# Kernel optimization log

Measured on AMD Instinct MI355X. Metric: run time of the kernel, lower is better.

## Reference

```python
import jax, jax.numpy as jnp
import numpy as np

# ---------------- irreps metadata: list of (mul, l, parity) ----------------
IR_A  = [(1, 0, 1)]                                        # '0e' input scalars
IR_B  = [(10,0,1),(10,0,-1),(10,0,1),(5,1,1),(5,1,-1)]     # Gate input, dim 60
IR_C  = [(10,0,1),(10,0,-1),(5,1,1),(5,1,-1)]              # Gate output, dim 50
IR_D  = [(1,0,-1),(6,0,1)]                                 # '0o + 6x0e', dim 7
IR_SH = [(1,0,1),(1,1,-1)]                                 # '0e + 1o'
CONVS = [(IR_A,IR_B),(IR_C,IR_B),(IR_C,IR_B),(IR_C,IR_B),(IR_C,IR_D)]
R_BASIS  = 2
DIAMETER = 5.0   # source used 1.5 -> degenerate 1^3 kernel; enlarged to exercise the steerable conv
STEP     = 1.0

def irdim(ir):
    return sum(m*(2*l+1) for m,l,_ in ir)

def irslices(ir):
    out, o = [], 0
    for m,l,_ in ir:
        d = m*(2*l+1); out.append(slice(o,o+d)); o += d
    return out

# normalized Clebsch-Gordan (wigner3j * sqrt(2*l_out+1)) for l<=1
_eps = np.zeros((3,3,3))
for a,b,c in [(0,1,2),(1,2,0),(2,0,1)]:
    _eps[a,b,c] = 1.0; _eps[b,a,c] = -1.0
CG = {
    (0,0,0): np.ones((1,1,1)),
    (0,1,1): np.eye(3).reshape(1,3,3),
    (1,0,1): np.eye(3).reshape(3,1,3),
    (1,1,0): (np.eye(3)/np.sqrt(3.0)).reshape(3,3,1),
    (1,1,1): _eps/np.sqrt(2.0),
}

def tp_ins(ir1, iro):
    ins = []
    for i1,(m1,l1,p1) in enumerate(ir1):
        for i2,(m2,l2,p2) in enumerate(IR_SH):
            for io,(mo,lo,po) in enumerate(iro):
                if po == p1*p2 and abs(l1-l2) <= lo <= l1+l2:
                    ins.append((i1,i2,io))
    return ins

def tp_numel(ir1, iro):
    return sum(R_BASIS*ir1[i1][0]*IR_SH[i2][0]*iro[io][0] for i1,i2,io in tp_ins(ir1,iro))

def lin_ins(ir1, iro):
    return [(i,j) for i,(m1,l1,p1) in enumerate(ir1)
                  for j,(m2,l2,p2) in enumerate(iro) if l1==l2 and p1==p2]

def lin_numel(ir1, iro):
    return sum(ir1[i][0]*iro[j][0] for i,j in lin_ins(ir1,iro))

def _lattice_features():
    # lattice offsets, smooth_finite radial basis (with cutoff) and SH ('0e+1o', component norm)
    r = DIAMETER/2.0
    s = int(np.floor(r/STEP))
    c = np.arange(-s, s+1, dtype=np.float64)*STEP
    lat = np.stack(np.meshgrid(c, c, c, indexing='ij'), -1)            # [K,K,K,3]
    d = np.linalg.norm(lat, axis=-1)
    vals = np.linspace(0.0, r, R_BASIS+2)[1:-1]
    step = vals[1]-vals[0]
    diff = (d[...,None]-vals)/step
    sus = lambda t: np.where(t>0, np.exp(-1.0/np.where(t>0, t, 1.0)), 0.0)
    emb = 1.14136*np.exp(2.0)*sus(diff+1.0)*sus(1.0-diff)              # [K,K,K,R]
    unit = lat/np.maximum(d, 1e-9)[...,None]
    sh = np.concatenate([np.ones_like(d)[...,None],
                         np.sqrt(3.0)*unit[...,[1,2,0]]], -1)          # [K,K,K,4], e3nn (y,z,x) order
    return jnp.asarray(emb, jnp.float32), jnp.asarray(sh, jnp.float32)

EMB, SH = _lattice_features()

def build_kernel(ir_in, ir_out, tw, lw):
    sin, sout, ssh = irslices(ir_in), irslices(ir_out), irslices(IR_SH)
    K = EMB.shape[0]
    k = jnp.zeros((K, K, K, irdim(ir_in), irdim(ir_out)), jnp.float32)
    off = 0
    for i1,i2,io in tp_ins(ir_in, ir_out):
        m1,l1,_ = ir_in[i1]; m2,l2,_ = IR_SH[i2]; mo,lo,_ = ir_out[io]
        n = R_BASIS*m1*m2*mo
        w = tw[off:off+n].reshape(R_BASIS, m1, mo); off += n           # m2 == 1 for SH
        cg = jnp.asarray(CG[(l1,l2,lo)], jnp.float32)
        alpha = 1.0/np.sqrt(m1*m2*R_BASIS)
        shseg = SH[..., ssh[i2]]                                       # [K,K,K,2l2+1]
        blk = alpha*jnp.einsum('xyzr,ruw,xyzj,ijk->xyzuiwk', EMB, w, shseg, cg)
        k = k.at[:,:,:, sin[i1], sout[io]].add(
            blk.reshape(K, K, K, m1*(2*l1+1), mo*(2*lo+1)))
    # self-connection Linear at the kernel center (radial basis vanishes at r=0)
    M = jnp.zeros((irdim(ir_in), irdim(ir_out)), jnp.float32)
    off = 0
    for i,j in lin_ins(ir_in, ir_out):
        m1,l1,_ = ir_in[i]; mo,_,_ = ir_out[j]
        w = lw[off:off+m1*mo].reshape(m1, mo); off += m1*mo
        eye = jnp.eye(2*l1+1, dtype=jnp.float32)
        blk = (1.0/np.sqrt(m1))*jnp.einsum('uw,ik->uiwk', w, eye)
        M = M.at[sin[i], sout[j]].add(blk.reshape(m1*(2*l1+1), mo*(2*l1+1)))
    cc = K//2
    return k.at[cc, cc, cc].set(M)

def equiv_conv(x, k):
    return jax.lax.conv_general_dilated(x, k, (1,1,1), 'SAME',
        dimension_numbers=('NXYZC', 'XYZIO', 'NXYZC'))

def gate(y):
    # Gate('10x0e+10x0o', [gelu, tanh], '10x0e', [sigmoid], '5x1e+5x1o')
    s = jnp.concatenate([jax.nn.gelu(y[..., :10]), jnp.tanh(y[..., 10:20])], -1)
    g = jax.nn.sigmoid(y[..., 20:30])                                  # 10 gate scalars
    v = y[..., 30:60].reshape(y.shape[:-1]+(10,3))*g[..., None]        # gate 5x1e + 5x1o
    return jnp.concatenate([s, v.reshape(y.shape[:-1]+(30,))], -1)

def _forward(x, tws, lws):
    y = x
    for i,(a,b) in enumerate(CONVS):
        y = equiv_conv(y, build_kernel(a, b, tws[i], lws[i]))
        if i < len(CONVS)-1:
            y = gate(y)
    return jnp.sum(y, axis=(1, 2, 3))                                  # [B, 7]

def setup_inputs() -> dict:
    key = jax.random.key(0)
    ks = jax.random.split(key, 11)
    inp = {'x': jax.random.normal(ks[0], (2, 48, 48, 48, 1), jnp.float32)}
    for i,(a,b) in enumerate(CONVS):
        inp[f'tp_w{i}'] = jax.random.normal(ks[1+i], (tp_numel(a,b),), jnp.float32)
        inp[f'lin_w{i}'] = jax.random.normal(ks[6+i], (lin_numel(a,b),), jnp.float32)
    return inp

def reference(x, tp_w0, tp_w1, tp_w2, tp_w3, tp_w4,
              lin_w0, lin_w1, lin_w2, lin_w3, lin_w4):
    return _forward(x, [tp_w0, tp_w1, tp_w2, tp_w3, tp_w4],
                    [lin_w0, lin_w1, lin_w2, lin_w3, lin_w4])
```

## Files before the change

### kernel.cpp

```cpp
#include <hip/hip_runtime.h>
#include <hip/hip_bf16.h>
#include <math.h>


typedef __attribute__((ext_vector_type(8))) short bf16x8;
typedef __attribute__((ext_vector_type(4))) float f32x4;

struct TpPath { int off, ci, co, m1, l1, i2, mo, lo; float alpha; };
struct LinPath { int off, ci, co, m1, l, mo; float norm; };

__device__ __constant__ TpPath g_tp[19] = {
  {0,  0,  0, 1, 0, 0, 10, 0, 0.70710678f},
  {20, 0, 20, 1, 0, 0, 10, 0, 0.70710678f},
  {40, 0, 45, 1, 0, 1,  5, 1, 0.70710678f},
  {0,    0,  0, 10, 0, 0, 10, 0, 0.22360680f},
  {200,  0, 20, 10, 0, 0, 10, 0, 0.22360680f},
  {400,  0, 45, 10, 0, 1,  5, 1, 0.22360680f},
  {500, 10, 10, 10, 0, 0, 10, 0, 0.22360680f},
  {700, 10, 30, 10, 0, 1,  5, 1, 0.22360680f},
  {800, 20, 30,  5, 1, 0,  5, 1, 0.31622777f},
  {850, 20, 10,  5, 1, 1, 10, 0, 0.31622777f},
  {950, 20, 45,  5, 1, 1,  5, 1, 0.31622777f},
  {1000,35, 45,  5, 1, 0,  5, 1, 0.31622777f},
  {1050,35,  0,  5, 1, 1, 10, 0, 0.31622777f},
  {1150,35, 20,  5, 1, 1, 10, 0, 0.31622777f},
  {1250,35, 30,  5, 1, 1,  5, 1, 0.31622777f},
  {0,    0, 1, 10, 0, 0, 6, 0, 0.22360680f},
  {120, 10, 0, 10, 0, 0, 1, 0, 0.22360680f},
  {140, 20, 0,  5, 1, 1, 1, 0, 0.31622777f},
  {150, 35, 1,  5, 1, 1, 6, 0, 0.31622777f},
};

__device__ __constant__ LinPath g_lin[9] = {
  {0,  0,  0, 1, 0, 10, 1.0f},
  {10, 0, 20, 1, 0, 10, 1.0f},
  {0,   0,  0, 10, 0, 10, 0.31622777f},
  {100, 0, 20, 10, 0, 10, 0.31622777f},
  {200,10, 10, 10, 0, 10, 0.31622777f},
  {300,20, 30,  5, 1,  5, 0.44721360f},
  {325,35, 45,  5, 1,  5, 0.44721360f},
  {0,  0, 1, 10, 0, 6, 0.31622777f},
  {60,10, 0, 10, 0, 1, 0.31622777f},
};

__device__ inline float sus_f(float t) { return t > 0.f ? __expf(-1.f / t) : 0.f; }

__global__ void build_tp_kernel(const float* __restrict__ tw, float* __restrict__ kbuf,
                                int CIN, int COUT, int path_base) {
  TpPath p = g_tp[path_base + blockIdx.x];
  const int dl1 = 2 * p.l1 + 1, dlo = 2 * p.lo + 1;
  const int du = p.m1 * dl1, dw = p.mo * dlo;
  const int total = 125 * du * dw;
  const float C0 = 1.14136f * expf(2.0f);
  for (int e = threadIdx.x; e < total; e += blockDim.x) {
    int xyz = e / (du * dw);
    int rem = e % (du * dw);
    int ui = rem / dw, wk = rem % dw;
    int u = ui / dl1, i = ui % dl1;
    int w = wk / dlo, kk = wk % dlo;
    int kx = xyz / 25, ky = (xyz / 5) % 5, kz = xyz % 5;
    float cx = (float)(kx - 2), cy = (float)(ky - 2), cz = (float)(kz - 2);
    float d = sqrtf(cx * cx + cy * cy + cz * cz);
    float t = 1.2f * d;
    float e0 = C0 * sus_f(t) * sus_f(2.f - t);
    float e1 = C0 * sus_f(t - 1.f) * sus_f(3.f - t);
    float radial = e0 * tw[p.off + (0 * p.m1 + u) * p.mo + w] +
                   e1 * tw[p.off + (1 * p.m1 + u) * p.mo + w];
    float invd = (d > 0.f) ? 1.f / d : 0.f;
    const float s3 = 1.7320508f;
    float sh1[3] = { s3 * cy * invd, s3 * cz * invd, s3 * cx * invd };
    float shfac;
    if (p.l1 == 0 && p.i2 == 0)      shfac = 1.f;
    else if (p.l1 == 0)              shfac = sh1[kk];
    else if (p.i2 == 0)              shfac = (i == kk) ? 1.f : 0.f;
    else if (p.lo == 0)              shfac = sh1[i] * 0.57735027f;
    else {
      if (i == kk) shfac = 0.f;
      else {
        int j = 3 - i - kk;
        float sgn = (j == (i + 1) % 3) ? 1.f : -1.f;
        shfac = sgn * sh1[j] * 0.70710678f;
      }
    }
    kbuf[(size_t)(xyz * CIN + p.ci + ui) * COUT + p.co + wk] = p.alpha * radial * shfac;
  }
}

__global__ void set_center_kernel(const float* __restrict__ lw, float* __restrict__ kbuf,
                                  int CIN, int COUT, int lin_base, int nlin) {
  for (int l = 0; l < nlin; l++) {
    LinPath q = g_lin[lin_base + l];
    int dl = 2 * q.l + 1;
    int tot = q.m1 * q.mo * dl;
    for (int e = threadIdx.x; e < tot; e += blockDim.x) {
      int u = e / (q.mo * dl);
      int r = e % (q.mo * dl);
      int w = r / dl, ii = r % dl;
      kbuf[(size_t)(62 * CIN + q.ci + u * dl + ii) * COUT + q.co + w * dl + ii] =
          q.norm * lw[q.off + u * q.mo + w];
    }
  }
}

__global__ void convert_w(const float* __restrict__ kbuf, unsigned short* __restrict__ kwbT,
                          int CIN, int COUT) {
  int idx = blockIdx.x * 256 + threadIdx.x;
  if (idx >= 125 * 64 * 64) return;
  int tap = idx >> 12, co = (idx >> 6) & 63, ci = idx & 63;
  float v = (ci < CIN && co < COUT) ? kbuf[((size_t)tap * CIN + ci) * COUT + co] : 0.f;
  __hip_bfloat16 h = __float2bfloat16(v);
  kwbT[idx] = *(unsigned short*)&h;
}

__global__ void build_w0(const float* __restrict__ k0, unsigned short* __restrict__ wb0L) {
  int idx = blockIdx.x * 256 + threadIdx.x;
  if (idx >= 5 * 2 * 64 * 32) return;
  int k = idx & 31, co = (idx >> 5) & 63, mf = (idx >> 11) & 1, dxi = idx >> 12;
  float v = 0.f;
  if (co < 60) {
    if (mf == 0) {
      int dy = k >> 3, dz = k & 7;
      if (dz < 5) v = k0[(size_t)(((dxi * 5 + dy) * 5 + dz)) * 60 + co];
    } else {
      int kg = k >> 3, dz = k & 7;
      if (kg == 0 && dz < 5) v = k0[(size_t)(((dxi * 5 + 4) * 5 + dz)) * 60 + co];
    }
  }
  __hip_bfloat16 h = __float2bfloat16(v);
  wb0L[idx] = *(unsigned short*)&h;
}

__device__ inline float gelu_f(float x) {
  float inner = 0.79788456f * (x + 0.044715f * x * x * x);
  return 0.5f * x * (1.f + tanhf(inner));
}
__device__ inline float sigm_f(float x) { return 1.f / (1.f + __expf(-x)); }

__device__ inline void gate_tile(const float* my, unsigned int* myO, int z) {
#pragma unroll
  for (int p = 0; p < 25; p++) {
    float a0, a1;
    if (p < 5) {
      a0 = gelu_f(my[(2 * p) * 16 + z]);
      a1 = gelu_f(my[(2 * p + 1) * 16 + z]);
    } else if (p < 10) {
      a0 = tanhf(my[(2 * p) * 16 + z]);
      a1 = tanhf(my[(2 * p + 1) * 16 + z]);
    } else {
      int q0 = 2 * (p - 10), q1 = q0 + 1;
      a0 = my[(30 + q0) * 16 + z] * sigm_f(my[(20 + q0 / 3) * 16 + z]);
      a1 = my[(30 + q1) * 16 + z] * sigm_f(my[(20 + q1 / 3) * 16 + z]);
    }
    __hip_bfloat162 p2;
    p2.x = __float2bfloat16(a0);
    p2.y = __float2bfloat16(a1);
    myO[z * 32 + p] = *(unsigned int*)&p2;
  }
#pragma unroll
  for (int p = 25; p < 32; p++) myO[z * 32 + p] = 0u;
}

template <int NT>
__device__ inline void epilogue_gate(f32x4 (&acc)[3][NT], float* my,
                                     unsigned short* out_, int n, int x, int y,
                                     int l, int lm, int kg) {
  unsigned int* myO = (unsigned int*)(my + 1024);
#pragma unroll
  for (int zt = 0; zt < 3; zt++) {
#pragma unroll
    for (int nt = 0; nt < NT; nt++)
      *(f32x4*)(my + (lm + 16 * nt) * 16 + 4 * kg) = acc[zt][nt];
    if (l < 16) gate_tile(my, myO, l);
    unsigned int* gout = (unsigned int*)out_ +
        ((size_t)(((n * 48 + x) * 48 + y) * 48 + 16 * zt)) * 32;
#pragma unroll 1
    for (int e = l; e < 512; e += 64) gout[e] = myO[e];
  }
}

template <int CIN, int COUT, int MODE>
__global__ __launch_bounds__(512, 2)
void conv_mfma(const unsigned short* __restrict__ act, const short* __restrict__ kwbT,
               void* __restrict__ out_) {
  constexpr int NTH = (MODE == 0) ? 2 : 1;
  constexpr int KC = (CIN + 31) / 32;
  __shared__ __align__(16) unsigned int Albs[12 * 48 * 32];

  const int tid = threadIdx.x;
  const int l = tid & 63;
  const int w = tid >> 6;
  const int wp = w & 3;
  const int ch = w >> 2;
  const int lm = l & 15;
  const int kg = l >> 4;
  const int co_off = (MODE == 0) ? ch * 32 : 0;

  const int bid = blockIdx.x;
  const int yb = bid % 6;
  const int x = (bid / 6) % 48;
  const int n = bid / (6 * 48);

  f32x4 acc[2][3][NTH];
#pragma unroll
  for (int yy = 0; yy < 2; yy++)
#pragma unroll
    for (int zt = 0; zt < 3; zt++)
#pragma unroll
      for (int nt = 0; nt < NTH; nt++) acc[yy][zt][nt] = (f32x4){0.f, 0.f, 0.f, 0.f};

  for (int dxi = 0; dxi < 5; dxi++) {
    int xin = x + dxi - 2;
    if (xin < 0 || xin >= 48) continue;
    __syncthreads();
    for (int e = tid; e < 12 * 48 * 32; e += 512) {
      int yi = e / (48 * 32);
      int rem = e % (48 * 32);
      int zin = rem / 32, pi = rem % 32;
      int yin = 8 * yb + yi - 2;
      unsigned int val = 0;
      if (yin >= 0 && yin < 48) {
        const unsigned short* p = act +
            ((size_t)((n * 48 + xin) * 48 + yin) * 48 + zin) * 64 + 2 * pi;
        val = *(const unsigned int*)p;
      }
      int u = pi >> 2, j = pi & 3;
      Albs[(yi * 48 + zin) * 32 + ((((u ^ (zin & 7)) << 2) | j))] = val;
    }
    __syncthreads();

    if (MODE == 0 || w < 4) {
      const short* Albs_s = (const short*)Albs;
#pragma unroll 1
      for (int dy = 0; dy < 5; dy++) {
        const int tapbase = (dxi * 5 + dy) * 5;
#pragma unroll
        for (int dz = 0; dz < 5; dz++) {
          bf16x8 bfr[NTH * KC];
          {
            const short* wb_ = kwbT + ((size_t)(tapbase + dz) << 12) +
                               (co_off + lm) * 64 + kg * 8;
#pragma unroll
            for (int nt = 0; nt < NTH; nt++)
#pragma unroll
              for (int kc = 0; kc < KC; kc++)
                bfr[nt * KC + kc] = *(const bf16x8*)(wb_ + nt * 1024 + kc * 32);
          }
          bf16x8 afr[2][3][KC];
#pragma unroll
          for (int zt = 0; zt < 3; zt++) {
            const int zraw = 16 * zt + lm + dz - 2;
            const int zc = min(max(zraw, 0), 47);
            const bool zval = (zraw >= 0) && (zraw < 48);
#pragma unroll
            for (int yy = 0; yy < 2; yy++) {
              const int yrow = 2 * wp + yy + dy;
              const int rowoff = (yrow * 48 + zc) * 64;
#pragma unroll
              for (int kc = 0; kc < KC; kc++) {
                int u = (4 * kc + kg) ^ (zc & 7);
                bf16x8 v = *(const bf16x8*)(Albs_s + rowoff + u * 8);
                afr[yy][zt][kc] = zval ? v : (bf16x8)(short)0;
              }
            }
          }
#pragma unroll
          for (int yy = 0; yy < 2; yy++)
#pragma unroll
            for (int zt = 0; zt < 3; zt++)
#pragma unroll
              for (int nt = 0; nt < NTH; nt++)
#pragma unroll
                for (int kc = 0; kc < KC; kc++)
                  acc[yy][zt][nt] = __builtin_amdgcn_mfma_f32_16x16x32_bf16(
                      afr[yy][zt][kc], bfr[nt * KC + kc], acc[yy][zt][nt], 0, 0, 0);
        }
      }
    }
  }

  if constexpr (MODE == 0) {
    __syncthreads();
    float* base = (float*)Albs;
    int par = 0;
#pragma unroll
    for (int yy = 0; yy < 2; yy++) {
#pragma unroll
      for (int zt = 0; zt < 3; zt++) {
        float* my = base + par * 6144 + wp * 1536;
        unsigned int* myO = (unsigned int*)(my + 1024);
#pragma unroll
        for (int nt = 0; nt < NTH; nt++)
          *(f32x4*)(my + (co_off + lm + 16 * nt) * 16 + 4 * kg) = acc[yy][zt][nt];
        __syncthreads();
        if (ch == 0 && l < 16) gate_tile(my, myO, l);
        __syncthreads();
        unsigned int* gout = (unsigned int*)out_ +
            ((size_t)(((n * 48 + x) * 48 + (8 * yb + 2 * wp + yy)) * 48 + 16 * zt)) * 32;
#pragma unroll
        for (int q = 0; q < 4; q++)
          gout[ch * 256 + q * 64 + l] = myO[ch * 256 + q * 64 + l];
        par ^= 1;
      }
    }
  } else {
    if (w < 4) {
      float s = 0.f;
#pragma unroll
      for (int yy = 0; yy < 2; yy++)
#pragma unroll
        for (int zt = 0; zt < 3; zt++)
#pragma unroll
          for (int r = 0; r < 4; r++) s += acc[yy][zt][0][r];
      s += __shfl_xor(s, 16);
      s += __shfl_xor(s, 32);
      if (l < 7) atomicAdd(&((float*)out_)[n * 7 + l], s);
    }
  }
}

__global__ __launch_bounds__(256, 4)
void conv0_mfma(const float* __restrict__ in_, const short* __restrict__ wb0L,
                unsigned short* __restrict__ out_) {
  __shared__ float A0[8 * 72];
  __shared__ __align__(16) float outbuf0[4 * 1536];

  const int tid = threadIdx.x;
  const int l = tid & 63;
  const int w = tid >> 6;
  const int lm = l & 15;
  const int kg = l >> 4;
  const int yb = blockIdx.x % 12;
  const int x = (blockIdx.x / 12) % 48;
  const int n = blockIdx.x / (12 * 48);

  f32x4 acc[3][4];
#pragma unroll
  for (int zt = 0; zt < 3; zt++)
#pragma unroll
    for (int nt = 0; nt < 4; nt++) acc[zt][nt] = (f32x4){0.f, 0.f, 0.f, 0.f};

  for (int dxi = 0; dxi < 5; dxi++) {
    int xin = x + dxi - 2;
    if (xin < 0 || xin >= 48) continue;
    __syncthreads();
    for (int e = tid; e < 8 * 72; e += 256) {
      int yi = e / 72, zz = e % 72;
      int yin = 4 * yb + yi - 2, zin = zz - 2;
      A0[e] = (yin >= 0 && yin < 48 && zin >= 0 && zin < 48)
                  ? in_[(size_t)((n * 48 + xin) * 48 + yin) * 48 + zin] : 0.f;
    }
    __syncthreads();
#pragma unroll
    for (int mf = 0; mf < 2; mf++) {
      const short* wbp = wb0L + ((size_t)(dxi * 2 + mf) * 64 + lm) * 32 + kg * 8;
      bf16x8 bfr[4];
#pragma unroll
      for (int nt = 0; nt < 4; nt++) bfr[nt] = *(const bf16x8*)(wbp + nt * 16 * 32);
      const int row = mf ? (w + 4) : (w + kg);
#pragma unroll
      for (int zt = 0; zt < 3; zt++) {
        const float* ap = A0 + row * 72 + 16 * zt + lm;
        union { bf16x8 v; unsigned short s[8]; } af;
#pragma unroll
        for (int j = 0; j < 8; j++) {
          __hip_bfloat16 h = __float2bfloat16(ap[j]);
          af.s[j] = *(unsigned short*)&h;
        }
#pragma unroll
        for (int nt = 0; nt < 4; nt++)
          acc[zt][nt] = __builtin_amdgcn_mfma_f32_16x16x32_bf16(
              af.v, bfr[nt], acc[zt][nt], 0, 0, 0);
      }
    }
  }

  float* my = outbuf0 + w * 1536;
  epilogue_gate<4>(acc, my, out_, n, x, 4 * yb + w, l, lm, kg);
}

extern "C" void kernel_launch(void* const* d_in, const int* in_sizes, int n_in,
                              void* d_out, int out_size, void* d_ws, size_t ws_size,
                              hipStream_t stream) {
  const float* x   = (const float*)d_in[0];
  const float* tw0 = (const float*)d_in[1];
  const float* lw0 = (const float*)d_in[2];
  const float* tw1 = (const float*)d_in[3];
  const float* lw1 = (const float*)d_in[4];
  const float* tw2 = (const float*)d_in[5];
  const float* lw2 = (const float*)d_in[6];
  const float* tw3 = (const float*)d_in[7];
  const float* lw3 = (const float*)d_in[8];
  const float* tw4 = (const float*)d_in[9];
  const float* lw4 = (const float*)d_in[10];

  float* ws = (float*)d_ws;
  float* k0 = ws;
  float* k1 = k0 + 7500;
  float* k2 = k1 + 375000;
  float* k3 = k2 + 375000;
  float* k4 = k3 + 375000;
  unsigned short* actA = (unsigned short*)(ws + 1200000);
  unsigned short* actB = actA + 14155776;
  unsigned short* wb1 = (unsigned short*)(ws + 15360000);
  unsigned short* wb2 = wb1 + 512000;
  unsigned short* wb3 = wb2 + 512000;
  unsigned short* wb4 = wb3 + 512000;
  unsigned short* wb0L = wb4 + 512000;

  hipMemsetAsync(ws, 0, (size_t)1176250 * sizeof(float), stream);
  hipMemsetAsync(d_out, 0, (size_t)out_size * sizeof(float), stream);

  build_tp_kernel<<<3, 128, 0, stream>>>(tw0, k0, 1, 60, 0);
  build_tp_kernel<<<12, 128, 0, stream>>>(tw1, k1, 50, 60, 3);
  build_tp_kernel<<<12, 128, 0, stream>>>(tw2, k2, 50, 60, 3);
  build_tp_kernel<<<12, 128, 0, stream>>>(tw3, k3, 50, 60, 3);
  build_tp_kernel<<<4, 128, 0, stream>>>(tw4, k4, 50, 7, 15);
  set_center_kernel<<<1, 256, 0, stream>>>(lw0, k0, 1, 60, 0, 2);
  set_center_kernel<<<1, 256, 0, stream>>>(lw1, k1, 50, 60, 2, 5);
  set_center_kernel<<<1, 256, 0, stream>>>(lw2, k2, 50, 60, 2, 5);
  set_center_kernel<<<1, 256, 0, stream>>>(lw3, k3, 50, 60, 2, 5);
  set_center_kernel<<<1, 256, 0, stream>>>(lw4, k4, 50, 7, 7, 2);

  convert_w<<<2000, 256, 0, stream>>>(k1, wb1, 50, 60);
  convert_w<<<2000, 256, 0, stream>>>(k2, wb2, 50, 60);
  convert_w<<<2000, 256, 0, stream>>>(k3, wb3, 50, 60);
  convert_w<<<2000, 256, 0, stream>>>(k4, wb4, 50, 7);
  build_w0<<<80, 256, 0, stream>>>(k0, wb0L);

  const int grid0 = 2 * 48 * 12;
  const int grid  = 2 * 48 * 6;
  conv0_mfma<<<grid0, 256, 0, stream>>>(x, (const short*)wb0L, actA);
  conv_mfma<50, 60, 0><<<grid, 512, 0, stream>>>(actA, (const short*)wb1, actB);
  conv_mfma<50, 60, 0><<<grid, 512, 0, stream>>>(actB, (const short*)wb2, actA);
  conv_mfma<50, 60, 0><<<grid, 512, 0, stream>>>(actA, (const short*)wb3, actB);
  conv_mfma<50, 7, 1><<<grid, 512, 0, stream>>>(actB, (const short*)wb4, d_out);
}
```

Baseline: 2.275 ms.

## Prefetch next x-plane into registers with vector loads and swizzle epilogue LDS

The activation staging loop now uses precomputed 16-byte vector global loads held in registers. The next x-plane is prefetched while MFMAs run on the current plane in LDS, replacing the old per-dword load-then-store loop. The epilogue accumulator and gate-output LDS layouts are XOR-swizzled to reduce bank conflicts. This costs 36 extra VGPRs for the prefetch buffer plus precomputed offsets, which may hurt occupancy under launch_bounds(512,2).

```diff
diff --git a/kernel.cpp b/kernel.cpp
--- a/kernel.cpp
+++ b/kernel.cpp
@@ -5,6 +5,7 @@
 
 typedef __attribute__((ext_vector_type(8))) short bf16x8;
 typedef __attribute__((ext_vector_type(4))) float f32x4;
+typedef __attribute__((ext_vector_type(4))) unsigned int u32x4;
 
 struct TpPath { int off, ci, co, m1, l1, i2, mo, lo; float alpha; };
 struct LinPath { int off, ci, co, m1, l, mo; float norm; };
@@ -136,28 +137,36 @@
 }
 __device__ inline float sigm_f(float x) { return 1.f / (1.f + __expf(-x)); }
 
+__device__ inline int eidx(int c, int z) {
+  return c * 16 + ((((z >> 2) ^ (c & 3)) << 2) | (z & 3));
+}
+__device__ inline int oidx(int z, int p) { return z * 32 + (p ^ z); }
+__device__ inline int uidx(int e) {
+  return (e & ~31) | ((e & 31) ^ ((e >> 5) & 15));
+}
+
 __device__ inline void gate_tile(const float* my, unsigned int* myO, int z) {
 #pragma unroll
   for (int p = 0; p < 25; p++) {
     float a0, a1;
     if (p < 5) {
-      a0 = gelu_f(my[(2 * p) * 16 + z]);
-      a1 = gelu_f(my[(2 * p + 1) * 16 + z]);
+      a0 = gelu_f(my[eidx(2 * p, z)]);
+      a1 = gelu_f(my[eidx(2 * p + 1, z)]);
     } else if (p < 10) {
-      a0 = tanhf(my[(2 * p) * 16 + z]);
-      a1 = tanhf(my[(2 * p + 1) * 16 + z]);
+      a0 = tanhf(my[eidx(2 * p, z)]);
+      a1 = tanhf(my[eidx(2 * p + 1, z)]);
     } else {
       int q0 = 2 * (p - 10), q1 = q0 + 1;
-      a0 = my[(30 + q0) * 16 + z] * sigm_f(my[(20 + q0 / 3) * 16 + z]);
-      a1 = my[(30 + q1) * 16 + z] * sigm_f(my[(20 + q1 / 3) * 16 + z]);
+      a0 = my[eidx(30 + q0, z)] * sigm_f(my[eidx(20 + q0 / 3, z)]);
+      a1 = my[eidx(30 + q1, z)] * sigm_f(my[eidx(20 + q1 / 3, z)]);
     }
     __hip_bfloat162 p2;
     p2.x = __float2bfloat16(a0);
     p2.y = __float2bfloat16(a1);
-    myO[z * 32 + p] = *(unsigned int*)&p2;
-  }
-#pragma unroll
-  for (int p = 25; p < 32; p++) myO[z * 32 + p] = 0u;
+    myO[oidx(z, p)] = *(unsigned int*)&p2;
+  }
+#pragma unroll
+  for (int p = 25; p < 32; p++) myO[oidx(z, p)] = 0u;
 }
 
 template <int NT>
@@ -169,12 +178,12 @@
   for (int zt = 0; zt < 3; zt++) {
 #pragma unroll
     for (int nt = 0; nt < NT; nt++)
-      *(f32x4*)(my + (lm + 16 * nt) * 16 + 4 * kg) = acc[zt][nt];
+      *(f32x4*)(my + (lm + 16 * nt) * 16 + ((kg ^ (lm & 3)) << 2)) = acc[zt][nt];
     if (l < 16) gate_tile(my, myO, l);
     unsigned int* gout = (unsigned int*)out_ +
         ((size_t)(((n * 48 + x) * 48 + y) * 48 + 16 * zt)) * 32;
 #pragma unroll 1
-    for (int e = l; e < 512; e += 64) gout[e] = myO[e];
+    for (int e = l; e < 512; e += 64) gout[e] = myO[uidx(e)];
   }
 }
 
@@ -200,6 +209,20 @@
   const int x = (bid / 6) % 48;
   const int n = bid / (6 * 48);
 
+  int g_off[9]; bool g_ok[9]; int l_off[9];
+#pragma unroll
+  for (int i = 0; i < 9; i++) {
+    int e = tid + i * 512;
+    int yi = e / 384;
+    int rem = e % 384;
+    int zin = rem >> 3, u = rem & 7;
+    int yin = 8 * yb + yi - 2;
+    g_ok[i] = (yin >= 0) && (yin < 48);
+    int yc = min(max(yin, 0), 47);
+    g_off[i] = (yc * 48 + zin) * 64 + u * 8;
+    l_off[i] = (yi * 48 + zin) * 32 + ((u ^ (zin & 7)) << 2);
+  }
+
   f32x4 acc[2][3][NTH];
 #pragma unroll
   for (int yy = 0; yy < 2; yy++)
@@ -208,27 +231,30 @@
 #pragma unroll
       for (int nt = 0; nt < NTH; nt++) acc[yy][zt][nt] = (f32x4){0.f, 0.f, 0.f, 0.f};
 
-  for (int dxi = 0; dxi < 5; dxi++) {
-    int xin = x + dxi - 2;
-    if (xin < 0 || xin >= 48) continue;
+  u32x4 rg[9];
+  const int xlo = max(x - 2, 0), xhi = min(x + 2, 47);
+
+#define LOADP(xin_)                                                            \
+  {                                                                            \
+    const unsigned short* pb = act + (size_t)((n * 48 + (xin_)) * 2304) * 64;  \
+    _Pragma("unroll")                                                          \
+    for (int i = 0; i < 9; i++)                                                \
+      rg[i] = g_ok[i] ? *(const u32x4*)(pb + g_off[i])                         \
+                      : (u32x4){0u, 0u, 0u, 0u};                               \
+  }
+
+  LOADP(xlo);
+#pragma unroll 1
+  for (int xin = xlo; xin <= xhi; ++xin) {
     __syncthreads();
-    for (int e = tid; e < 12 * 48 * 32; e += 512) {
-      int yi = e / (48 * 32);
-      int rem = e % (48 * 32);
-      int zin = rem / 32, pi = rem % 32;
-      int yin = 8 * yb + yi - 2;
-      unsigned int val = 0;
-      if (yin >= 0 && yin < 48) {
-        const unsigned short* p = act +
-            ((size_t)((n * 48 + xin) * 48 + yin) * 48 + zin) * 64 + 2 * pi;
-        val = *(const unsigned int*)p;
-      }
-      int u = pi >> 2, j = pi & 3;
-      Albs[(yi * 48 + zin) * 32 + ((((u ^ (zin & 7)) << 2) | j))] = val;
-    }
+#pragma unroll
+    for (int i = 0; i < 9; i++)
+      *(u32x4*)((unsigned int*)Albs + l_off[i]) = rg[i];
     __syncthreads();
+    if (xin < xhi) LOADP(xin + 1);
 
     if (MODE == 0 || w < 4) {
+      const int dxi = xin - x + 2;
       const short* Albs_s = (const short*)Albs;
 #pragma unroll 1
       for (int dy = 0; dy < 5; dy++) {
@@ -277,6 +303,7 @@
       }
     }
   }
+#undef LOADP
 
   if constexpr (MODE == 0) {
     __syncthreads();
@@ -290,15 +317,18 @@
         unsigned int* myO = (unsigned int*)(my + 1024);
 #pragma unroll
         for (int nt = 0; nt < NTH; nt++)
-          *(f32x4*)(my + (co_off + lm + 16 * nt) * 16 + 4 * kg) = acc[yy][zt][nt];
+          *(f32x4*)(my + (co_off + lm + 16 * nt) * 16 + ((kg ^ (lm & 3)) << 2)) =
+              acc[yy][zt][nt];
         __syncthreads();
         if (ch == 0 && l < 16) gate_tile(my, myO, l);
         __syncthreads();
         unsigned int* gout = (unsigned int*)out_ +
             ((size_t)(((n * 48 + x) * 48 + (8 * yb + 2 * wp + yy)) * 48 + 16 * zt)) * 32;
 #pragma unroll
-        for (int q = 0; q < 4; q++)
-          gout[ch * 256 + q * 64 + l] = myO[ch * 256 + q * 64 + l];
+        for (int q = 0; q < 4; q++) {
+          int e = ch * 256 + q * 64 + l;
+          gout[e] = myO[uidx(e)];
+        }
         par ^= 1;
       }
     }
```

Measured after the change: 1.987 ms. -12.7%, faster.
